# Performance work log

Hardware: AMD Instinct MI355X
Metric: run time of the kernel (lower is better)

## Reference

```python
import jax, jax.numpy as jnp
import numpy as np

# ---- static config (mirrors TritonMoEConfig) ----
N_EMBD = 1024
EXPERT_SIZES = [(4, 1024), (4, 2048)]  # (count, width) pairs
TOP_K = 2                              # num_active_experts
B, S = 1, 2048

WIDTHS = []
for count, size in EXPERT_SIZES:
    WIDTHS += [size] * count
OFFSETS = np.concatenate([[0], np.cumsum(WIDTHS)]).astype(np.int64)
E = len(WIDTHS)                 # 8 experts
TOTAL_W = int(OFFSETS[-1])      # 12288
MAX_W = max(WIDTHS)             # 2048


def setup_inputs() -> dict:
    key = jax.random.key(0)
    k1, k2, k3, k4 = jax.random.split(key, 4)
    x = jax.random.normal(k1, (B, S, N_EMBD), jnp.float32)
    # router: nn.Linear(n_embd, num_experts, bias=False) -> weight [E, d]
    router_w = jax.random.normal(k2, (E, N_EMBD), jnp.float32) * 0.02
    # trunc_normal(std=0.02, a=-0.06, b=0.06) == truncated_normal(-3,3)*0.02
    w1 = jax.random.truncated_normal(k3, -3.0, 3.0, (N_EMBD, TOTAL_W), jnp.float32) * 0.02
    w2 = jax.random.truncated_normal(k4, -3.0, 3.0, (TOTAL_W, N_EMBD), jnp.float32) * 0.02
    return {"x": x, "router_w": router_w, "w1": w1, "w2": w2}


def _stack_experts(w1, w2):
    # Slice the flat concatenated weights into per-expert blocks, zero-padded
    # to MAX_W. Zero pad is exact: relu(x@0)^2 == 0 and padded w2 rows are 0.
    W1e, W2e = [], []
    for e in range(E):  # fixed small loop over structurally distinct experts
        off, wd = int(OFFSETS[e]), WIDTHS[e]
        pad = MAX_W - wd
        W1e.append(jnp.pad(w1[:, off:off + wd], ((0, 0), (0, pad))))
        W2e.append(jnp.pad(w2[off:off + wd, :], ((0, pad), (0, 0))))
    return jnp.stack(W1e), jnp.stack(W2e)  # [E,d,maxw], [E,maxw,d]


def reference(x, router_w, w1, w2):
    b, s, d = x.shape
    xf = x.reshape(-1, d)  # [T, d]
    # routing: sigmoid probs (fp32), top-k, renormalize
    logits = xf @ router_w.T  # [T, E]
    probs = jax.nn.sigmoid(logits.astype(jnp.float32))
    topw, sel = jax.lax.top_k(probs, TOP_K)  # [T, K]
    topw = topw / (topw.sum(-1, keepdims=True) + 1e-20)
    topw = topw.astype(x.dtype)
    # combine[t, e] = sum_k topw[t,k] * (sel[t,k] == e)
    onehot = (sel[:, :, None] == jnp.arange(E)[None, None, :])
    combine = jnp.sum(topw[:, :, None] * onehot, axis=1)  # [T, E]
    # expert MLP with relu_squared activation; combine zeros unselected experts
    W1e, W2e = _stack_experts(w1, w2)
    h = jnp.einsum('td,edw->tew', xf, W1e)   # up-proj, [T,E,maxw]
    h = jnp.square(jax.nn.relu(h))           # relu_squared
    y = jnp.einsum('tew,ewd->ted', h, W2e)   # down-proj, [T,E,d]
    out = jnp.einsum('ted,te->td', y, combine)
    return out.reshape(b, s, d)
```

## Files before the change

### kernel.cpp

```cpp
#include <hip/hip_runtime.h>
#include <hip/hip_bf16.h>

#define T_TOKENS 2048
#define D_EMBD   1024
#define N_EXP    8
#define TOTAL_W  12288
#define CAP      2048
#define CAPH     2048

typedef __attribute__((ext_vector_type(8))) short bf16x8;
typedef __attribute__((ext_vector_type(4))) float f32x4;
typedef __attribute__((ext_vector_type(4))) unsigned short u16x4;
typedef __attribute__((ext_vector_type(8))) unsigned short u16x8;

__device__ __constant__ int d_OFF[N_EXP] = {0,1024,2048,3072,4096,6144,8192,10240};
__device__ __constant__ int d_WID[N_EXP] = {1024,1024,1024,1024,2048,2048,2048,2048};

#define WS_TOK   1024
#define WS_SLK   (WS_TOK + N_EXP*CAP*4)
#define WS_WGT   (WS_SLK + N_EXP*CAP*4)
#define WS_WG2   (WS_WGT + N_EXP*CAP*4)
#define WS_XB    (WS_WG2 + T_TOKENS*2*4)
#define WS_W1B   (WS_XB + T_TOKENS*D_EMBD*2)
#define WS_W2B   (WS_W1B + D_EMBD*TOTAL_W*2)
#define WS_H     (WS_W2B + (size_t)TOTAL_W*D_EMBD*2)
#define WS_END   (WS_H + (size_t)TOTAL_W*CAPH*2)
#define WS_Y     WS_XB

__device__ __forceinline__ void gload_lds16(const void* g, void* l) {
    __builtin_amdgcn_global_load_lds(
        (const __attribute__((address_space(1))) void*)g,
        (__attribute__((address_space(3))) void*)l, 16, 0, 0);
}

__device__ __forceinline__ unsigned short f2bf(float f) {
    __hip_bfloat16 h = __float2bfloat16(f);
    return *reinterpret_cast<unsigned short*>(&h);
}

__global__ __launch_bounds__(64) void zero_kernel(int* __restrict__ cnt) {
    if (threadIdx.x < N_EXP) cnt[threadIdx.x << 5] = 0;
}

__device__ __forceinline__ void router_body(
    int rb, int tid, char* smem,
    const float* __restrict__ x, const float* __restrict__ rw,
    int* __restrict__ cnt, int* __restrict__ tok, int* __restrict__ slotk,
    float* __restrict__ wgtl, float* __restrict__ wgt2,
    __hip_bfloat16* __restrict__ xb)
{
    int*   lcnt  = (int*)smem;
    int*   lbase = (int*)(smem + 32);
    int   (*ltok)[32] = (int(*)[32])(smem + 64);
    float (*lwgt)[32] = (float(*)[32])(smem + 64 + 1024);
    int   (*lkk)[32]  = (int(*)[32])(smem + 64 + 2048);

    const int wv = tid >> 6, lane = tid & 63;
    if (tid < N_EXP) lcnt[tid] = 0;
    __syncthreads();

    const float4* x4  = (const float4*)x;
    const float4* rw4 = (const float4*)rw;
    for (int ts = 0; ts < 8; ++ts) {
        const int t = rb * 32 + wv * 8 + ts;
        float4 xv[4];
#pragma unroll
        for (int i = 0; i < 4; ++i) xv[i] = x4[(size_t)t * 256 + lane + 64 * i];

        if (xb) {
#pragma unroll
            for (int i = 0; i < 4; ++i) {
                u16x4 o;
                o[0] = f2bf(xv[i].x); o[1] = f2bf(xv[i].y);
                o[2] = f2bf(xv[i].z); o[3] = f2bf(xv[i].w);
                *reinterpret_cast<u16x4*>(xb + (size_t)t * D_EMBD + (lane + 64 * i) * 4) = o;
            }
        }

        float acc[N_EXP];
#pragma unroll
        for (int e = 0; e < N_EXP; ++e) {
            float a = 0.f;
#pragma unroll
            for (int i = 0; i < 4; ++i) {
                float4 w4 = rw4[e * 256 + lane + 64 * i];
                a += xv[i].x * w4.x + xv[i].y * w4.y + xv[i].z * w4.z + xv[i].w * w4.w;
            }
            acc[e] = a;
        }
#pragma unroll
        for (int e = 0; e < N_EXP; ++e)
#pragma unroll
            for (int o = 32; o > 0; o >>= 1) acc[e] += __shfl_xor(acc[e], o, 64);

        if (lane == 0) {
            float p[N_EXP];
#pragma unroll
            for (int e = 0; e < N_EXP; ++e) p[e] = 1.f / (1.f + __expf(-acc[e]));
            int e0 = 0;
#pragma unroll
            for (int e = 1; e < N_EXP; ++e) if (p[e] > p[e0]) e0 = e;
            int e1 = (e0 == 0) ? 1 : 0;
#pragma unroll
            for (int e = 0; e < N_EXP; ++e) if (e != e0 && p[e] > p[e1]) e1 = e;
            float w0 = p[e0], w1 = p[e1], s = w0 + w1 + 1e-20f;
            int s0 = atomicAdd(&lcnt[e0], 1);
            ltok[e0][s0] = t;  lwgt[e0][s0] = w0 / s;  lkk[e0][s0] = 0;
            int s1 = atomicAdd(&lcnt[e1], 1);
            ltok[e1][s1] = t;  lwgt[e1][s1] = w1 / s;  lkk[e1][s1] = 1;
        }
    }
    __syncthreads();
    if (tid < N_EXP) lbase[tid] = atomicAdd(&cnt[tid << 5], lcnt[tid]);
    __syncthreads();
    {
        const int e = tid >> 5, i = tid & 31;
        if (i < lcnt[e]) {
            int dst = e * CAP + lbase[e] + i;
            int t   = ltok[e][i], k = lkk[e][i];
            tok[dst]   = t;
            wgtl[dst]  = lwgt[e][i];
            slotk[dst] = t * 2 + k;
            wgt2[t * 2 + k] = lwgt[e][i];
        }
    }
}

__device__ __forceinline__ void transpose4_body(
    const float* __restrict__ in, __hip_bfloat16* __restrict__ out,
    int R, int C, int br0, int bc, int tid, char* smem)
{
    float (*ls)[65] = (float(*)[65])smem;
    const int c0 = bc << 6;
#pragma unroll
    for (int s = 0; s < 4; ++s) {
        const int r0 = (br0 + s) << 6;
        if (s) __syncthreads();
#pragma unroll
        for (int i = 0; i < 4; ++i) {
            int flat = i * 1024 + tid * 4;
            int r = flat >> 6, c = flat & 63;
            float4 v = *reinterpret_cast<const float4*>(&in[(size_t)(r0 + r) * C + c0 + c]);
            ls[r][c] = v.x; ls[r][c + 1] = v.y; ls[r][c + 2] = v.z; ls[r][c + 3] = v.w;
        }
        __syncthreads();
#pragma unroll
        for (int i = 0; i < 2; ++i) {
            int flat = i * 2048 + tid * 8;
            int cc = flat >> 6, rr = flat & 63;
            u16x8 o;
#pragma unroll
            for (int q = 0; q < 8; ++q) o[q] = f2bf(ls[rr + q][cc]);
            *reinterpret_cast<u16x8*>(&out[(size_t)(c0 + cc) * R + r0 + rr]) = o;
        }
    }
}

__global__ __launch_bounds__(256) void prep4_kernel(
    const float* __restrict__ x, const float* __restrict__ rw,
    const float* __restrict__ w1, const float* __restrict__ w2,
    int* __restrict__ cnt, int* __restrict__ tok, int* __restrict__ slotk,
    float* __restrict__ wgtl, float* __restrict__ wgt2,
    __hip_bfloat16* __restrict__ xb, __hip_bfloat16* __restrict__ w1b,
    __hip_bfloat16* __restrict__ w2b)
{
    __shared__ __align__(16) char smem[16640];
    const int bx = blockIdx.x, tid = threadIdx.x;
    if (bx < 64) {
        router_body(bx, tid, smem, x, rw, cnt, tok, slotk, wgtl, wgt2, xb);
    } else if (bx < 832) {
        int tb = bx - 64;
        transpose4_body(w1, w1b, D_EMBD, TOTAL_W, (tb & 3) * 4, tb >> 2, tid, smem);
    } else {
        int tb = bx - 832;
        transpose4_body(w2, w2b, TOTAL_W, D_EMBD, (tb % 48) * 4, tb / 48, tid, smem);
    }
}

__global__ __launch_bounds__(256) void router2_kernel(
    const float* __restrict__ x, const float* __restrict__ rw,
    int* __restrict__ cnt, int* __restrict__ tok, int* __restrict__ slotk,
    float* __restrict__ wgtl, float* __restrict__ wgt2)
{
    __shared__ __align__(16) char smem[16640];
    router_body(blockIdx.x, threadIdx.x, smem, x, rw, cnt, tok, slotk, wgtl, wgt2,
                ((__hip_bfloat16*)0));
}

__global__ __launch_bounds__(256) void gemm1_kernel(
    const char* __restrict__ xb, const char* __restrict__ w1b,
    const int* __restrict__ cnt, const int* __restrict__ tok,
    __hip_bfloat16* __restrict__ H)
{
    int bx0 = blockIdx.x;
    int bx = (bx0 & 7) * 384 + (bx0 >> 3);
    int e, tt, nT;
    if (bx < 2048) {
        e = 4 + (bx >> 9); int r = bx & 511; tt = r >> 4; nT = r & 15;
    } else {
        int b2 = bx - 2048; e = b2 >> 8; int r = b2 & 255; tt = r >> 3; nT = r & 7;
    }
    const int nt = cnt[e << 5];
    if (tt * 64 >= nt) return;

    const int we  = d_WID[e];
    const int n0  = nT * 128;
    const int tid = threadIdx.x;
    const int wv  = tid >> 6, lane = tid & 63;
    const int wr  = wv >> 1, wc = wv & 1;

    __shared__ __align__(16) char lds[2][24576];
    __shared__ int ts_s[64];

    if (tid < 64) {
        int s = tt * 64 + tid;
        ts_s[tid] = (s < nt) ? tok[e * CAP + s] : 0;
    }
    __syncthreads();

    f32x4 acc[2][4];
#pragma unroll
    for (int mi = 0; mi < 2; ++mi)
#pragma unroll
        for (int nj = 0; nj < 4; ++nj) acc[mi][nj] = (f32x4){0.f,0.f,0.f,0.f};

    const char* w1row = w1b + (size_t)(d_OFF[e] + n0) * 2048;

    auto STAGE = [&](int buf, int ks) {
        const int k0b = ks * 128;
#pragma unroll
        for (int j = 0; j < 6; ++j) {
            const int flat = j * 4096 + tid * 16;
            char* dst = lds[buf] + flat;
            if (flat < 8192) {
                int r = flat >> 7, cb = flat & 127;
                gload_lds16(xb + (size_t)ts_s[r] * 2048 + k0b + (cb ^ ((r & 7) << 4)), dst);
            } else {
                int f2 = flat - 8192, n = f2 >> 7, cb = f2 & 127;
                gload_lds16(w1row + (size_t)n * 2048 + k0b + (cb ^ ((n & 7) << 4)), dst);
            }
        }
    };
    auto COMPUTE = [&](int buf) {
        const char* LA = lds[buf];
        const char* LB = lds[buf] + 8192;
#pragma unroll
        for (int ksl = 0; ksl < 2; ++ksl) {
            const int kb = ksl * 64 + (lane >> 4) * 16;
            bf16x8 a[2], b[4];
#pragma unroll
            for (int mi = 0; mi < 2; ++mi) {
                int row = wr * 32 + mi * 16 + (lane & 15);
                a[mi] = *(const bf16x8*)(LA + row * 128 + (kb ^ ((row & 7) << 4)));
            }
#pragma unroll
            for (int nj = 0; nj < 4; ++nj) {
                int n = wc * 64 + nj * 16 + (lane & 15);
                b[nj] = *(const bf16x8*)(LB + n * 128 + (kb ^ ((n & 7) << 4)));
            }
#pragma unroll
            for (int mi = 0; mi < 2; ++mi)
#pragma unroll
                for (int nj = 0; nj < 4; ++nj)
                    acc[mi][nj] = __builtin_amdgcn_mfma_f32_16x16x32_bf16(
                        a[mi], b[nj], acc[mi][nj], 0, 0, 0);
        }
    };

    STAGE(0, 0);
    int cur = 0;
    for (int ks = 0; ks < 16; ++ks) {
        if (ks + 1 < 16) {
            STAGE(cur ^ 1, ks + 1);
            asm volatile("s_waitcnt vmcnt(6)" ::: "memory");
        } else {
            asm volatile("s_waitcnt vmcnt(0)" ::: "memory");
        }
        __builtin_amdgcn_s_barrier();
        __builtin_amdgcn_sched_barrier(0);
        COMPUTE(cur);
        __builtin_amdgcn_sched_barrier(0);
        __builtin_amdgcn_s_barrier();
        cur ^= 1;
    }

    const size_t hbase = (size_t)d_OFF[e] * CAPH;
#pragma unroll
    for (int mi = 0; mi < 2; ++mi)
#pragma unroll
        for (int q = 0; q < 4; ++q) {
            int row  = wr * 32 + mi * 16 + (lane >> 4) * 4 + q;
            int slot = tt * 64 + row;
            __hip_bfloat16* hp = H + hbase + (size_t)slot * we + n0 + wc * 64 + (lane & 15);
#pragma unroll
            for (int nj = 0; nj < 4; ++nj) {
                float v = fmaxf(acc[mi][nj][q], 0.f);
                hp[nj * 16] = __float2bfloat16(v * v);
            }
        }
}

__global__ __launch_bounds__(256) void gemm2_kernel(
    const char* __restrict__ Hb, const char* __restrict__ w2b,
    const int* __restrict__ cnt, const int* __restrict__ slotk,
    float* __restrict__ Y)
{
    int bx0 = blockIdx.x;
    int bx = (bx0 & 7) * 256 + (bx0 >> 3);
    int e, tt, nT;
    if (bx < 1024) {
        e = 4 + (bx >> 8); int r = bx & 255; tt = r >> 3; nT = r & 7;
    } else {
        int b2 = bx - 1024; e = b2 >> 8; int r = b2 & 255; tt = r >> 3; nT = r & 7;
    }
    const int nt = cnt[e << 5];
    if (tt * 64 >= nt) return;

    const int we  = d_WID[e];
    const int n0  = nT * 128;
    const int tid = threadIdx.x;
    const int wv  = tid >> 6, lane = tid & 63;
    const int wr  = wv >> 1, wc = wv & 1;

    __shared__ __align__(16) char lds[2][24576];
    __shared__ int yk_s[64];

    if (tid < 64) {
        int s = tt * 64 + tid;
        yk_s[tid] = (s < nt) ? slotk[e * CAP + s] : 0;
    }
    __syncthreads();

    f32x4 acc[2][4];
#pragma unroll
    for (int mi = 0; mi < 2; ++mi)
#pragma unroll
        for (int nj = 0; nj < 4; ++nj) acc[mi][nj] = (f32x4){0.f,0.f,0.f,0.f};

    const char* Habase = Hb + ((size_t)d_OFF[e] * CAPH + (size_t)tt * 64 * we) * 2;
    const char* w2base = w2b + ((size_t)n0 * TOTAL_W + d_OFF[e]) * 2;
    const int   ksteps = we >> 6;

    auto STAGE = [&](int buf, int ks) {
        const int k0b = ks * 128;
#pragma unroll
        for (int j = 0; j < 6; ++j) {
            const int flat = j * 4096 + tid * 16;
            char* dst = lds[buf] + flat;
            if (flat < 8192) {
                int r = flat >> 7, cb = flat & 127;
                gload_lds16(Habase + (size_t)r * (we * 2) + k0b + (cb ^ ((r & 7) << 4)), dst);
            } else {
                int f2 = flat - 8192, n = f2 >> 7, cb = f2 & 127;
                gload_lds16(w2base + (size_t)n * (TOTAL_W * 2) + k0b + (cb ^ ((n & 7) << 4)), dst);
            }
        }
    };
    auto COMPUTE = [&](int buf) {
        const char* LA = lds[buf];
        const char* LB = lds[buf] + 8192;
#pragma unroll
        for (int ksl = 0; ksl < 2; ++ksl) {
            const int kb = ksl * 64 + (lane >> 4) * 16;
            bf16x8 a[2], b[4];
#pragma unroll
            for (int mi = 0; mi < 2; ++mi) {
                int row = wr * 32 + mi * 16 + (lane & 15);
                a[mi] = *(const bf16x8*)(LA + row * 128 + (kb ^ ((row & 7) << 4)));
            }
#pragma unroll
            for (int nj = 0; nj < 4; ++nj) {
                int n = wc * 64 + nj * 16 + (lane & 15);
                b[nj] = *(const bf16x8*)(LB + n * 128 + (kb ^ ((n & 7) << 4)));
            }
#pragma unroll
            for (int mi = 0; mi < 2; ++mi)
#pragma unroll
                for (int nj = 0; nj < 4; ++nj)
                    acc[mi][nj] = __builtin_amdgcn_mfma_f32_16x16x32_bf16(
                        a[mi], b[nj], acc[mi][nj], 0, 0, 0);
        }
    };

    STAGE(0, 0);
    int cur = 0;
    for (int ks = 0; ks < ksteps; ++ks) {
        if (ks + 1 < ksteps) {
            STAGE(cur ^ 1, ks + 1);
            asm volatile("s_waitcnt vmcnt(6)" ::: "memory");
        } else {
            asm volatile("s_waitcnt vmcnt(0)" ::: "memory");
        }
        __builtin_amdgcn_s_barrier();
        __builtin_amdgcn_sched_barrier(0);
        COMPUTE(cur);
        __builtin_amdgcn_sched_barrier(0);
        __builtin_amdgcn_s_barrier();
        cur ^= 1;
    }

#pragma unroll
    for (int mi = 0; mi < 2; ++mi)
#pragma unroll
        for (int q = 0; q < 4; ++q) {
            int row  = wr * 32 + mi * 16 + (lane >> 4) * 4 + q;
            int slot = tt * 64 + row;
            if (slot < nt) {
                float* yp = Y + (size_t)yk_s[row] * D_EMBD + n0 + wc * 64 + (lane & 15);
#pragma unroll
                for (int nj = 0; nj < 4; ++nj)
                    yp[nj * 16] = acc[mi][nj][q];
            }
        }
}

__global__ __launch_bounds__(256) void gather_kernel(
    const float* __restrict__ Y, const float* __restrict__ wgt2,
    float* __restrict__ out)
{
    const int t = blockIdx.x, tid = threadIdx.x;
    const float w0 = wgt2[t * 2], w1 = wgt2[t * 2 + 1];
    const float4 y0 = reinterpret_cast<const float4*>(Y + (size_t)(t * 2) * D_EMBD)[tid];
    const float4 y1 = reinterpret_cast<const float4*>(Y + (size_t)(t * 2 + 1) * D_EMBD)[tid];
    float4 o;
    o.x = w0 * y0.x + w1 * y1.x;  o.y = w0 * y0.y + w1 * y1.y;
    o.z = w0 * y0.z + w1 * y1.z;  o.w = w0 * y0.w + w1 * y1.w;
    reinterpret_cast<float4*>(out + (size_t)t * D_EMBD)[tid] = o;
}

__global__ __launch_bounds__(256, 3) void moe_group_kernel(
    const float* __restrict__ x, const float* __restrict__ w1,
    const float* __restrict__ w2, const int* __restrict__ cnt,
    const int* __restrict__ tok, const float* __restrict__ wgtl,
    float* __restrict__ out)
{
    int e, tt, colh, wh, nwh;
    int bx = blockIdx.x;
    if (bx < 1024) { e = bx >> 8; int rem = bx & 255; wh = rem & 1; colh = (rem >> 1) & 1; tt = rem >> 2; nwh = 2; }
    else { int b2 = bx - 1024; e = 4 + (b2 >> 9); int rem = b2 & 511; wh = rem & 3; colh = (rem >> 2) & 1; tt = rem >> 3; nwh = 4; }
    const int nt = cnt[e << 5];
    if (tt * 32 >= nt) return;

    const int tid = threadIdx.x;
    const int off = d_OFF[e];
    const int wtn = d_WID[e] >> 7;
    const int wpb = wtn / nwh;
    const int wt0 = wh * wpb;

    __shared__ float xs[128][36];
    __shared__ float hs[128][36];
    __shared__ int   ts_s[32];
    __shared__ float wg_s[32];

    if (tid < 32) {
        int s = tt * 32 + tid;
        ts_s[tid] = (s < nt) ? tok[e * CAP + s] : 0;
        wg_s[tid] = (s < nt) ? wgtl[e * CAP + s] : 0.f;
    }

    const int tg = tid >> 5, cg = tid & 31;
    float acc_dn[4][16];
#pragma unroll
    for (int a = 0; a < 4; ++a)
#pragma unroll
        for (int m = 0; m < 16; ++m) acc_dn[a][m] = 0.f;

    for (int wt = wt0; wt < wt0 + wpb; ++wt) {
        float au[4][4];
#pragma unroll
        for (int a = 0; a < 4; ++a)
#pragma unroll
            for (int b = 0; b < 4; ++b) au[a][b] = 0.f;
        const int cw1 = off + wt * 128 + cg * 4;
        for (int dc = 0; dc < 8; ++dc) {
            const int d0 = dc * 128;
            __syncthreads();
#pragma unroll
            for (int r = 0; r < 16; ++r) {
                int flat = r * 256 + tid, ii = flat & 127, t = flat >> 7;
                xs[ii][t] = x[(size_t)ts_s[t] * D_EMBD + d0 + ii];
            }
            __syncthreads();
            const float* pw = w1 + (size_t)d0 * TOTAL_W + cw1;
            for (int ii = 0; ii < 128; ++ii) {
                const float4 xv = *reinterpret_cast<const float4*>(&xs[ii][tg * 4]);
                const float4 wv = *reinterpret_cast<const float4*>(pw);
                pw += TOTAL_W;
                const float xa[4] = {xv.x, xv.y, xv.z, xv.w};
                const float wb[4] = {wv.x, wv.y, wv.z, wv.w};
#pragma unroll
                for (int a = 0; a < 4; ++a)
#pragma unroll
                    for (int b = 0; b < 4; ++b) au[a][b] += xa[a] * wb[b];
            }
        }
#pragma unroll
        for (int b = 0; b < 4; ++b) {
            float4 v;
            float r0 = fmaxf(au[0][b], 0.f), r1 = fmaxf(au[1][b], 0.f);
            float r2 = fmaxf(au[2][b], 0.f), r3 = fmaxf(au[3][b], 0.f);
            v.x = r0 * r0; v.y = r1 * r1; v.z = r2 * r2; v.w = r3 * r3;
            *reinterpret_cast<float4*>(&hs[cg * 4 + b][tg * 4]) = v;
        }
        __syncthreads();
        const float* pw2 = w2 + (size_t)(off + wt * 128) * D_EMBD + colh * 512 + cg * 4;
        for (int j = 0; j < 128; ++j) {
            const float4 hv = *reinterpret_cast<const float4*>(&hs[j][tg * 4]);
            const float ha[4] = {hv.x, hv.y, hv.z, hv.w};
            const float* row = pw2 + (size_t)j * D_EMBD;
#pragma unroll
            for (int b = 0; b < 4; ++b) {
                const float4 wv = *reinterpret_cast<const float4*>(row + b * 128);
                const float wq[4] = {wv.x, wv.y, wv.z, wv.w};
#pragma unroll
                for (int a = 0; a < 4; ++a)
#pragma unroll
                    for (int q = 0; q < 4; ++q)
                        acc_dn[a][b * 4 + q] += ha[a] * wq[q];
            }
        }
        __syncthreads();
    }
#pragma unroll
    for (int a = 0; a < 4; ++a) {
        const int   t  = ts_s[tg * 4 + a];
        const float wg = wg_s[tg * 4 + a];
        float* ot = out + (size_t)t * D_EMBD + colh * 512 + cg * 4;
#pragma unroll
        for (int b = 0; b < 4; ++b)
#pragma unroll
            for (int q = 0; q < 4; ++q)
                atomicAdd(&ot[b * 128 + q], wg * acc_dn[a][b * 4 + q]);
    }
}

extern "C" void kernel_launch(void* const* d_in, const int* in_sizes, int n_in,
                              void* d_out, int out_size, void* d_ws, size_t ws_size,
                              hipStream_t stream) {
    const float* x  = (const float*)d_in[0];
    const float* rw = (const float*)d_in[1];
    const float* w1 = (const float*)d_in[2];
    const float* w2 = (const float*)d_in[3];
    float* out = (float*)d_out;

    char*  ws    = (char*)d_ws;
    int*   cnt   = (int*)ws;
    int*   tokl  = (int*)(ws + WS_TOK);
    int*   slotk = (int*)(ws + WS_SLK);
    float* wgtl  = (float*)(ws + WS_WGT);
    float* wgt2  = (float*)(ws + WS_WG2);

    if (ws_size >= WS_END) {
        __hip_bfloat16* xb  = (__hip_bfloat16*)(ws + WS_XB);
        __hip_bfloat16* w1b = (__hip_bfloat16*)(ws + WS_W1B);
        __hip_bfloat16* w2b = (__hip_bfloat16*)(ws + WS_W2B);
        __hip_bfloat16* H   = (__hip_bfloat16*)(ws + WS_H);
        float*          Y   = (float*)(ws + WS_Y);

        zero_kernel<<<1, 64, 0, stream>>>(cnt);
        prep4_kernel<<<1600, 256, 0, stream>>>(x, rw, w1, w2, cnt, tokl, slotk, wgtl, wgt2,
                                               xb, w1b, w2b);
        gemm1_kernel<<<3072, 256, 0, stream>>>((const char*)xb, (const char*)w1b, cnt, tokl, H);
        gemm2_kernel<<<2048, 256, 0, stream>>>((const char*)H, (const char*)w2b, cnt, slotk, Y);
        gather_kernel<<<T_TOKENS, 256, 0, stream>>>(Y, wgt2, out);
    } else {
        hipMemsetAsync(d_ws, 0, 1024, stream);
        hipMemsetAsync(d_out, 0, (size_t)out_size * sizeof(float), stream);
        router2_kernel<<<T_TOKENS / 32, 256, 0, stream>>>(x, rw, cnt, tokl, slotk, wgtl, wgt2);
        moe_group_kernel<<<1024 + 2048, 256, 0, stream>>>(x, w1, w2, cnt, tokl, wgtl, out);
    }
}
```

Baseline: 109.8 us.

## Use two-wave GEMM blocks with 64x64 warp tiles and finer transpose blocks

Both grouped GEMM kernels drop from four waves to two per block. Each wave now computes a 64x64 output tile (4x4 MFMA accumulators) instead of 32x64, and does twice the staging loads per step. This raises per-wave register reuse of the A fragments and lowers waves per block, at the cost of more accumulator registers and less latency hiding inside each block. The weight transpose prep also switches from 4 tiles per block to 1 tile per block, using four times as many blocks, which trades loop work per block for more parallelism.

New measurement: 123.9 us. 1.13x slower.

```diff
diff --git a/kernel.cpp b/kernel.cpp
--- a/kernel.cpp
+++ b/kernel.cpp
@@ -126,37 +126,32 @@
     }
 }
 
-__device__ __forceinline__ void transpose4_body(
+__device__ __forceinline__ void transpose_body(
     const float* __restrict__ in, __hip_bfloat16* __restrict__ out,
-    int R, int C, int br0, int bc, int tid, char* smem)
+    int R, int C, int br, int bc, int tid, char* smem)
 {
     float (*ls)[65] = (float(*)[65])smem;
-    const int c0 = bc << 6;
-#pragma unroll
-    for (int s = 0; s < 4; ++s) {
-        const int r0 = (br0 + s) << 6;
-        if (s) __syncthreads();
-#pragma unroll
-        for (int i = 0; i < 4; ++i) {
-            int flat = i * 1024 + tid * 4;
-            int r = flat >> 6, c = flat & 63;
-            float4 v = *reinterpret_cast<const float4*>(&in[(size_t)(r0 + r) * C + c0 + c]);
-            ls[r][c] = v.x; ls[r][c + 1] = v.y; ls[r][c + 2] = v.z; ls[r][c + 3] = v.w;
-        }
-        __syncthreads();
-#pragma unroll
-        for (int i = 0; i < 2; ++i) {
-            int flat = i * 2048 + tid * 8;
-            int cc = flat >> 6, rr = flat & 63;
-            u16x8 o;
-#pragma unroll
-            for (int q = 0; q < 8; ++q) o[q] = f2bf(ls[rr + q][cc]);
-            *reinterpret_cast<u16x8*>(&out[(size_t)(c0 + cc) * R + r0 + rr]) = o;
-        }
-    }
-}
-
-__global__ __launch_bounds__(256) void prep4_kernel(
+    const int r0 = br << 6, c0 = bc << 6;
+#pragma unroll
+    for (int i = 0; i < 4; ++i) {
+        int flat = i * 1024 + tid * 4;
+        int r = flat >> 6, c = flat & 63;
+        float4 v = *reinterpret_cast<const float4*>(&in[(size_t)(r0 + r) * C + c0 + c]);
+        ls[r][c] = v.x; ls[r][c + 1] = v.y; ls[r][c + 2] = v.z; ls[r][c + 3] = v.w;
+    }
+    __syncthreads();
+#pragma unroll
+    for (int i = 0; i < 2; ++i) {
+        int flat = i * 2048 + tid * 8;
+        int cc = flat >> 6, rr = flat & 63;
+        u16x8 o;
+#pragma unroll
+        for (int q = 0; q < 8; ++q) o[q] = f2bf(ls[rr + q][cc]);
+        *reinterpret_cast<u16x8*>(&out[(size_t)(c0 + cc) * R + r0 + rr]) = o;
+    }
+}
+
+__global__ __launch_bounds__(256) void prep5_kernel(
     const float* __restrict__ x, const float* __restrict__ rw,
     const float* __restrict__ w1, const float* __restrict__ w2,
     int* __restrict__ cnt, int* __restrict__ tok, int* __restrict__ slotk,
@@ -168,12 +163,12 @@
     const int bx = blockIdx.x, tid = threadIdx.x;
     if (bx < 64) {
         router_body(bx, tid, smem, x, rw, cnt, tok, slotk, wgtl, wgt2, xb);
-    } else if (bx < 832) {
+    } else if (bx < 3136) {
         int tb = bx - 64;
-        transpose4_body(w1, w1b, D_EMBD, TOTAL_W, (tb & 3) * 4, tb >> 2, tid, smem);
+        transpose_body(w1, w1b, D_EMBD, TOTAL_W, tb / 192, tb % 192, tid, smem);
     } else {
-        int tb = bx - 832;
-        transpose4_body(w2, w2b, TOTAL_W, D_EMBD, (tb % 48) * 4, tb / 48, tid, smem);
+        int tb = bx - 3136;
+        transpose_body(w2, w2b, TOTAL_W, D_EMBD, tb / 16, tb % 16, tid, smem);
     }
 }
 
@@ -187,7 +182,7 @@
                 ((__hip_bfloat16*)0));
 }
 
-__global__ __launch_bounds__(256) void gemm1_kernel(
+__global__ __launch_bounds__(128) void gemm1_kernel(
     const char* __restrict__ xb, const char* __restrict__ w1b,
     const int* __restrict__ cnt, const int* __restrict__ tok,
     __hip_bfloat16* __restrict__ H)
@@ -207,7 +202,6 @@
     const int n0  = nT * 128;
     const int tid = threadIdx.x;
     const int wv  = tid >> 6, lane = tid & 63;
-    const int wr  = wv >> 1, wc = wv & 1;
 
     __shared__ __align__(16) char lds[2][24576];
     __shared__ int ts_s[64];
@@ -218,9 +212,9 @@
     }
     __syncthreads();
 
-    f32x4 acc[2][4];
-#pragma unroll
-    for (int mi = 0; mi < 2; ++mi)
+    f32x4 acc[4][4];
+#pragma unroll
+    for (int mi = 0; mi < 4; ++mi)
 #pragma unroll
         for (int nj = 0; nj < 4; ++nj) acc[mi][nj] = (f32x4){0.f,0.f,0.f,0.f};
 
@@ -229,8 +223,8 @@
     auto STAGE = [&](int buf, int ks) {
         const int k0b = ks * 128;
 #pragma unroll
-        for (int j = 0; j < 6; ++j) {
-            const int flat = j * 4096 + tid * 16;
+        for (int j = 0; j < 12; ++j) {
+            const int flat = j * 2048 + tid * 16;
             char* dst = lds[buf] + flat;
             if (flat < 8192) {
                 int r = flat >> 7, cb = flat & 127;
@@ -247,19 +241,19 @@
 #pragma unroll
         for (int ksl = 0; ksl < 2; ++ksl) {
             const int kb = ksl * 64 + (lane >> 4) * 16;
-            bf16x8 a[2], b[4];
-#pragma unroll
-            for (int mi = 0; mi < 2; ++mi) {
-                int row = wr * 32 + mi * 16 + (lane & 15);
+            bf16x8 a[4], b[4];
+#pragma unroll
+            for (int mi = 0; mi < 4; ++mi) {
+                int row = mi * 16 + (lane & 15);
                 a[mi] = *(const bf16x8*)(LA + row * 128 + (kb ^ ((row & 7) << 4)));
             }
 #pragma unroll
             for (int nj = 0; nj < 4; ++nj) {
-                int n = wc * 64 + nj * 16 + (lane & 15);
+                int n = wv * 64 + nj * 16 + (lane & 15);
                 b[nj] = *(const bf16x8*)(LB + n * 128 + (kb ^ ((n & 7) << 4)));
             }
 #pragma unroll
-            for (int mi = 0; mi < 2; ++mi)
+            for (int mi = 0; mi < 4; ++mi)
 #pragma unroll
                 for (int nj = 0; nj < 4; ++nj)
                     acc[mi][nj] = __builtin_amdgcn_mfma_f32_16x16x32_bf16(
@@ -272,7 +266,7 @@
     for (int ks = 0; ks < 16; ++ks) {
         if (ks + 1 < 16) {
             STAGE(cur ^ 1, ks + 1);
-            asm volatile("s_waitcnt vmcnt(6)" ::: "memory");
+            asm volatile("s_waitcnt vmcnt(12)" ::: "memory");
         } else {
             asm volatile("s_waitcnt vmcnt(0)" ::: "memory");
         }
@@ -286,12 +280,12 @@
 
     const size_t hbase = (size_t)d_OFF[e] * CAPH;
 #pragma unroll
-    for (int mi = 0; mi < 2; ++mi)
+    for (int mi = 0; mi < 4; ++mi)
 #pragma unroll
         for (int q = 0; q < 4; ++q) {
-            int row  = wr * 32 + mi * 16 + (lane >> 4) * 4 + q;
+            int row  = mi * 16 + (lane >> 4) * 4 + q;
             int slot = tt * 64 + row;
-            __hip_bfloat16* hp = H + hbase + (size_t)slot * we + n0 + wc * 64 + (lane & 15);
+            __hip_bfloat16* hp = H + hbase + (size_t)slot * we + n0 + wv * 64 + (lane & 15);
 #pragma unroll
             for (int nj = 0; nj < 4; ++nj) {
                 float v = fmaxf(acc[mi][nj][q], 0.f);
@@ -300,7 +294,7 @@
         }
 }
 
-__global__ __launch_bounds__(256) void gemm2_kernel(
+__global__ __launch_bounds__(128) void gemm2_kernel(
     const char* __restrict__ Hb, const char* __restrict__ w2b,
     const int* __restrict__ cnt, const int* __restrict__ slotk,
     float* __restrict__ Y)
@@ -320,7 +314,6 @@
     const int n0  = nT * 128;
     const int tid = threadIdx.x;
     const int wv  = tid >> 6, lane = tid & 63;
-    const int wr  = wv >> 1, wc = wv & 1;
 
     __shared__ __align__(16) char lds[2][24576];
     __shared__ int yk_s[64];
@@ -331,9 +324,9 @@
     }
     __syncthreads();
 
-    f32x4 acc[2][4];
-#pragma unroll
-    for (int mi = 0; mi < 2; ++mi)
+    f32x4 acc[4][4];
+#pragma unroll
+    for (int mi = 0; mi < 4; ++mi)
 #pragma unroll
         for (int nj = 0; nj < 4; ++nj) acc[mi][nj] = (f32x4){0.f,0.f,0.f,0.f};
 
@@ -344,8 +337,8 @@
     auto STAGE = [&](int buf, int ks) {
         const int k0b = ks * 128;
 #pragma unroll
-        for (int j = 0; j < 6; ++j) {
-            const int flat = j * 4096 + tid * 16;
+        for (int j = 0; j < 12; ++j) {
+            const int flat = j * 2048 + tid * 16;
             char* dst = lds[buf] + flat;
             if (flat < 8192) {
                 int r = flat >> 7, cb = flat & 127;
@@ -362,19 +355,19 @@
 #pragma unroll
         for (int ksl = 0; ksl < 2; ++ksl) {
             const int kb = ksl * 64 + (lane >> 4) * 16;
-            bf16x8 a[2], b[4];
-#pragma unroll
-            for (int mi = 0; mi < 2; ++mi) {
-                int row = wr * 32 + mi * 16 + (lane & 15);
+            bf16x8 a[4], b[4];
+#pragma unroll
+            for (int mi = 0; mi < 4; ++mi) {
+                int row = mi * 16 + (lane & 15);
                 a[mi] = *(const bf16x8*)(LA + row * 128 + (kb ^ ((row & 7) << 4)));
             }
 #pragma unroll
             for (int nj = 0; nj < 4; ++nj) {
-                int n = wc * 64 + nj * 16 + (lane & 15);
+                int n = wv * 64 + nj * 16 + (lane & 15);
                 b[nj] = *(const bf16x8*)(LB + n * 128 + (kb ^ ((n & 7) << 4)));
             }
 #pragma unroll
-            for (int mi = 0; mi < 2; ++mi)
+            for (int mi = 0; mi < 4; ++mi)
 #pragma unroll
                 for (int nj = 0; nj < 4; ++nj)
                     acc[mi][nj] = __builtin_amdgcn_mfma_f32_16x16x32_bf16(
@@ -387,7 +380,7 @@
     for (int ks = 0; ks < ksteps; ++ks) {
         if (ks + 1 < ksteps) {
             STAGE(cur ^ 1, ks + 1);
-            asm volatile("s_waitcnt vmcnt(6)" ::: "memory");
+            asm volatile("s_waitcnt vmcnt(12)" ::: "memory");
         } else {
             asm volatile("s_waitcnt vmcnt(0)" ::: "memory");
         }
@@ -400,13 +393,13 @@
     }
 
 #pragma unroll
-    for (int mi = 0; mi < 2; ++mi)
+    for (int mi = 0; mi < 4; ++mi)
 #pragma unroll
         for (int q = 0; q < 4; ++q) {
-            int row  = wr * 32 + mi * 16 + (lane >> 4) * 4 + q;
+            int row  = mi * 16 + (lane >> 4) * 4 + q;
             int slot = tt * 64 + row;
             if (slot < nt) {
-                float* yp = Y + (size_t)yk_s[row] * D_EMBD + n0 + wc * 64 + (lane & 15);
+                float* yp = Y + (size_t)yk_s[row] * D_EMBD + n0 + wv * 64 + (lane & 15);
 #pragma unroll
                 for (int nj = 0; nj < 4; ++nj)
                     yp[nj * 16] = acc[mi][nj][q];
@@ -558,10 +551,10 @@
         float*          Y   = (float*)(ws + WS_Y);
 
         zero_kernel<<<1, 64, 0, stream>>>(cnt);
-        prep4_kernel<<<1600, 256, 0, stream>>>(x, rw, w1, w2, cnt, tokl, slotk, wgtl, wgt2,
+        prep5_kernel<<<6208, 256, 0, stream>>>(x, rw, w1, w2, cnt, tokl, slotk, wgtl, wgt2,
                                                xb, w1b, w2b);
-        gemm1_kernel<<<3072, 256, 0, stream>>>((const char*)xb, (const char*)w1b, cnt, tokl, H);
-        gemm2_kernel<<<2048, 256, 0, stream>>>((const char*)H, (const char*)w2b, cnt, slotk, Y);
+        gemm1_kernel<<<3072, 128, 0, stream>>>((const char*)xb, (const char*)w1b, cnt, tokl, H);
+        gemm2_kernel<<<2048, 128, 0, stream>>>((const char*)H, (const char*)w2b, cnt, slotk, Y);
         gather_kernel<<<T_TOKENS, 256, 0, stream>>>(Y, wgt2, out);
     } else {
         hipMemsetAsync(d_ws, 0, 1024, stream);
```
